# Performance work log

Hardware: AMD Instinct MI355X
Metric: run time of the kernel (lower is better)

## Reference

```python
import jax, jax.numpy as jnp
import numpy as np

EPS = 1e-6
NUM_HEADS = 16

def _phi(x):
    # elu kernel feature map: elu(x) + 1 (ensures positivity)
    return jax.nn.elu(x) + 1.0

def setup_inputs() -> dict:
    key = jax.random.key(0)
    ks = jax.random.split(key, 5)
    B, S, D = 2, 2048, 1024
    scale = 1.0 / np.sqrt(D)  # mimic xavier-ish magnitude
    return {
        "x": jax.random.normal(ks[0], (B, S, D), dtype=jnp.float32),
        "Wq": jax.random.normal(ks[1], (D, D), dtype=jnp.float32) * scale,
        "bq": jnp.zeros((D,), dtype=jnp.float32),
        "Wk": jax.random.normal(ks[2], (D, D), dtype=jnp.float32) * scale,
        "bk": jnp.zeros((D,), dtype=jnp.float32),
        "Wv": jax.random.normal(ks[3], (D, D), dtype=jnp.float32) * scale,
        "bv": jnp.zeros((D,), dtype=jnp.float32),
        "Wo": jax.random.normal(ks[4], (D, D), dtype=jnp.float32) * scale,
        "bo": jnp.zeros((D,), dtype=jnp.float32),
    }

def reference(x, Wq, bq, Wk, bk, Wv, bv, Wo, bo):
    B, S, D = x.shape
    H = NUM_HEADS
    hd = D // H
    # projections (torch Linear: x @ W.T + b)
    q = (x @ Wq.T + bq).reshape(B, S, H, hd).transpose(0, 2, 1, 3)  # [B,H,S,d]
    k = (x @ Wk.T + bk).reshape(B, S, H, hd).transpose(0, 2, 1, 3)
    v = (x @ Wv.T + bv).reshape(B, S, H, hd).transpose(0, 2, 1, 3)
    q = _phi(q)
    k = _phi(k)
    # prefix sums of outer products k_t v_t^T and of k_t (causal linear attention)
    kv_cum = jnp.cumsum(k[..., :, None] * v[..., None, :], axis=2)  # [B,H,S,d,d]
    k_cum = jnp.cumsum(k, axis=2)                                   # [B,H,S,d]
    num = jnp.einsum('bhsd,bhsde->bhse', q, kv_cum)                 # [B,H,S,d]
    den = jnp.einsum('bhsd,bhsd->bhs', q, k_cum)                    # [B,H,S]
    out = num / (den[..., None] + EPS)
    out = out.transpose(0, 2, 1, 3).reshape(B, S, D)
    return out @ Wo.T + bo
```

## Files before the change

### kernel.cpp

```cpp
#include <hip/hip_runtime.h>

typedef unsigned short u16;
typedef __attribute__((ext_vector_type(8))) short bf16x8;
typedef __attribute__((ext_vector_type(4))) float f32x4;

#define DEVI static __device__ __forceinline__

DEVI u16 f2bf(float f) {
  union { float f; unsigned int u; } a; a.f = f;
  unsigned int u = a.u;
  u += 0x7fffu + ((u >> 16) & 1u);
  return (u16)(u >> 16);
}
DEVI float bf2f(u16 h) {
  union { unsigned int u; float f; } a; a.u = ((unsigned int)h) << 16;
  return a.f;
}

DEVI void gload_lds16(const u16* g, u16* l) {
  __builtin_amdgcn_global_load_lds(
      (const __attribute__((address_space(1))) void*)g,
      (__attribute__((address_space(3))) void*)l, 16, 0, 0);
}

DEVI int ldsIdx(int row, int col) {
  return ((col >> 5) << 11) + (row << 5) + (col & 31);
}

struct alignas(8) US4 { u16 a, b, c, d; };

__global__ __launch_bounds__(256) void k_cvt(const float* __restrict__ s,
                                             u16* __restrict__ d, int n4) {
  int i = blockIdx.x * 256 + threadIdx.x;
  if (i >= n4) return;
  f32x4 v = ((const f32x4*)s)[i];
  US4 o{f2bf(v[0]), f2bf(v[1]), f2bf(v[2]), f2bf(v[3])};
  ((US4*)d)[i] = o;
}

__global__ __launch_bounds__(256) void k_gemm_qkv(
    const u16* __restrict__ A, const u16* __restrict__ W,
    const float* __restrict__ bq, const float* __restrict__ bk,
    const float* __restrict__ bv, u16* __restrict__ qb, u16* __restrict__ kb,
    u16* __restrict__ ktb, u16* __restrict__ vtb) {
  __shared__ __align__(16) u16 As[128 * 32];
  __shared__ __align__(16) u16 Bs[128 * 32];
  const int tid = threadIdx.x;
  const int lane = tid & 63;
  const int wave = tid >> 6;
  const int wm = wave >> 1, wn = wave & 1;
  const int m0 = blockIdx.x * 128, n0 = blockIdx.y * 128;
  const int K = 1024;

  f32x4 acc[4][4];
#pragma unroll
  for (int i = 0; i < 4; i++)
#pragma unroll
    for (int j = 0; j < 4; j++) acc[i][j] = (f32x4){0.f, 0.f, 0.f, 0.f};

  const int r0 = tid >> 2, c0 = (tid & 3) * 8;
  const int r1 = (tid + 256) >> 2;
  const u16* Ab0 = A + (size_t)(m0 + r0) * K + c0;
  const u16* Ab1 = A + (size_t)(m0 + r1) * K + c0;
  const u16* Bb0 = W + (size_t)(n0 + r0) * K + c0;
  const u16* Bb1 = W + (size_t)(n0 + r1) * K + c0;
  u16* lA0 = &As[tid * 8];
  u16* lA1 = &As[(tid + 256) * 8];
  u16* lB0 = &Bs[tid * 8];
  u16* lB1 = &Bs[(tid + 256) * 8];

  for (int k0 = 0; k0 < K; k0 += 32) {
    __syncthreads();
    gload_lds16(Ab0 + k0, lA0);
    gload_lds16(Ab1 + k0, lA1);
    gload_lds16(Bb0 + k0, lB0);
    gload_lds16(Bb1 + k0, lB1);
    __syncthreads();
    const int koff = (lane >> 4) * 8;
    bf16x8 af[4], bfr[4];
#pragma unroll
    for (int t = 0; t < 4; t++) {
      af[t] = *(const bf16x8*)&As[(wm * 64 + t * 16 + (lane & 15)) * 32 + koff];
      bfr[t] = *(const bf16x8*)&Bs[(wn * 64 + t * 16 + (lane & 15)) * 32 + koff];
    }
#pragma unroll
    for (int i = 0; i < 4; i++)
#pragma unroll
      for (int j = 0; j < 4; j++)
        acc[i][j] = __builtin_amdgcn_mfma_f32_16x16x32_bf16(af[i], bfr[j],
                                                            acc[i][j], 0, 0, 0);
  }

  const int lr = (lane >> 4) * 4, lc = lane & 15;
  const int region = (int)(blockIdx.y >> 3);
  const float* bias = region == 0 ? bq : (region == 1 ? bk : bv);
#pragma unroll
  for (int j = 0; j < 4; j++) {
    const int colg = n0 + wn * 64 + j * 16 + lc;
    const int cl = colg - (region << 10);
    const float bvv = bias[cl];
#pragma unroll
    for (int i = 0; i < 4; i++) {
      const int row0 = m0 + wm * 64 + i * 16 + lr;
      float v4[4];
#pragma unroll
      for (int r = 0; r < 4; r++) {
        float v = acc[i][j][r] + bvv;
        if (region < 2) v = (v > 0.f) ? (v + 1.f) : __expf(v);
        v4[r] = v;
      }
      if (region == 0) {
#pragma unroll
        for (int r = 0; r < 4; r++)
          qb[(size_t)(row0 + r) * 1024 + cl] = f2bf(v4[r]);
      } else if (region == 1) {
#pragma unroll
        for (int r = 0; r < 4; r++)
          kb[(size_t)(row0 + r) * 1024 + cl] = f2bf(v4[r]);
        US4 o{f2bf(v4[0]), f2bf(v4[1]), f2bf(v4[2]), f2bf(v4[3])};
        *(US4*)&ktb[(size_t)cl * 4096 + row0] = o;
      } else {
        US4 o{f2bf(v4[0]), f2bf(v4[1]), f2bf(v4[2]), f2bf(v4[3])};
        *(US4*)&vtb[(size_t)cl * 4096 + row0] = o;
      }
    }
  }
}

__global__ __launch_bounds__(256) void k_gemm_out(const u16* __restrict__ A,
                                                  const u16* __restrict__ B,
                                                  const float* __restrict__ bias,
                                                  float* __restrict__ C, int M,
                                                  int N, int K) {
  __shared__ __align__(16) u16 As[128 * 32];
  __shared__ __align__(16) u16 Bs[128 * 32];
  const int tid = threadIdx.x;
  const int lane = tid & 63;
  const int wave = tid >> 6;
  const int wm = wave >> 1, wn = wave & 1;
  const int m0 = blockIdx.x * 128, n0 = blockIdx.y * 128;

  f32x4 acc[4][4];
#pragma unroll
  for (int i = 0; i < 4; i++)
#pragma unroll
    for (int j = 0; j < 4; j++) acc[i][j] = (f32x4){0.f, 0.f, 0.f, 0.f};

  const int r0 = tid >> 2, c0 = (tid & 3) * 8;
  const int r1 = (tid + 256) >> 2;
  const u16* Ab0 = A + (size_t)(m0 + r0) * K + c0;
  const u16* Ab1 = A + (size_t)(m0 + r1) * K + c0;
  const u16* Bb0 = B + (size_t)(n0 + r0) * K + c0;
  const u16* Bb1 = B + (size_t)(n0 + r1) * K + c0;
  u16* lA0 = &As[tid * 8];
  u16* lA1 = &As[(tid + 256) * 8];
  u16* lB0 = &Bs[tid * 8];
  u16* lB1 = &Bs[(tid + 256) * 8];

  for (int k0 = 0; k0 < K; k0 += 32) {
    __syncthreads();
    gload_lds16(Ab0 + k0, lA0);
    gload_lds16(Ab1 + k0, lA1);
    gload_lds16(Bb0 + k0, lB0);
    gload_lds16(Bb1 + k0, lB1);
    __syncthreads();
    const int koff = (lane >> 4) * 8;
    bf16x8 af[4], bfr[4];
#pragma unroll
    for (int t = 0; t < 4; t++) {
      af[t] = *(const bf16x8*)&As[(wm * 64 + t * 16 + (lane & 15)) * 32 + koff];
      bfr[t] = *(const bf16x8*)&Bs[(wn * 64 + t * 16 + (lane & 15)) * 32 + koff];
    }
#pragma unroll
    for (int i = 0; i < 4; i++)
#pragma unroll
      for (int j = 0; j < 4; j++)
        acc[i][j] = __builtin_amdgcn_mfma_f32_16x16x32_bf16(af[i], bfr[j],
                                                            acc[i][j], 0, 0, 0);
  }

  const int lr = (lane >> 4) * 4, lc = lane & 15;
#pragma unroll
  for (int j = 0; j < 4; j++) {
    const int col = n0 + wn * 64 + j * 16 + lc;
    const float bv = bias[col];
#pragma unroll
    for (int i = 0; i < 4; i++) {
      const int row = m0 + wm * 64 + i * 16 + lr;
#pragma unroll
      for (int r = 0; r < 4; r++)
        C[(size_t)(row + r) * N + col] = acc[i][j][r] + bv;
    }
  }
}

__global__ __launch_bounds__(256) void k_chunk2(const u16* __restrict__ ktb,
                                                const u16* __restrict__ vtb,
                                                float* __restrict__ KVt,
                                                float* __restrict__ Ks) {
  __shared__ __align__(16) u16 Kt[4096];
  __shared__ __align__(16) u16 Vt[4096];
  __shared__ float ksp[64][4];
  const int tid = threadIdx.x, lane = tid & 63, wave = tid >> 6;
  const int ci = blockIdx.x, h = blockIdx.y, b = blockIdx.z;
  const int t0 = b * 2048 + ci * 64, dB = h * 64;
  const int c = (b * 16 + h) * 32 + ci;
  const int row = tid >> 2, colr = (tid & 3) * 8;
#pragma unroll
  for (int r = 0; r < 2; r++) {
    const int col = r * 32 + colr;
    gload_lds16(ktb + (size_t)(dB + row) * 4096 + t0 + col, Kt + r * 2048 + tid * 8);
    gload_lds16(vtb + (size_t)(dB + row) * 4096 + t0 + col, Vt + r * 2048 + tid * 8);
  }
  __syncthreads();
  {
    const int rr = tid >> 2, part = tid & 3;
    float s = 0.f;
#pragma unroll
    for (int t = 0; t < 16; t++) s += bf2f(Kt[ldsIdx(rr, part * 16 + t)]);
    ksp[rr][part] = s;
  }
  __syncthreads();
  if (tid < 64)
    Ks[c * 64 + tid] = ksp[tid][0] + ksp[tid][1] + ksp[tid][2] + ksp[tid][3];

  const int wm = wave >> 1, wn = wave & 1;
  const int md0 = wm * 32, ne0 = wn * 32;
  const int m = lane & 15, quad = lane >> 4;
  f32x4 acc[2][2];
#pragma unroll
  for (int i = 0; i < 2; i++)
#pragma unroll
    for (int j = 0; j < 2; j++) acc[i][j] = (f32x4){0.f, 0.f, 0.f, 0.f};
#pragma unroll
  for (int ks = 0; ks < 2; ks++) {
    const int koff = ks * 32 + quad * 8;
    bf16x8 af[2], bfr[2];
#pragma unroll
    for (int i = 0; i < 2; i++)
      af[i] = *(const bf16x8*)&Kt[ldsIdx(md0 + i * 16 + m, koff)];
#pragma unroll
    for (int j = 0; j < 2; j++)
      bfr[j] = *(const bf16x8*)&Vt[ldsIdx(ne0 + j * 16 + m, koff)];
#pragma unroll
    for (int i = 0; i < 2; i++)
#pragma unroll
      for (int j = 0; j < 2; j++)
        acc[i][j] = __builtin_amdgcn_mfma_f32_16x16x32_bf16(af[i], bfr[j],
                                                            acc[i][j], 0, 0, 0);
  }
  float* out = KVt + (size_t)c * 4096;
#pragma unroll
  for (int i = 0; i < 2; i++)
#pragma unroll
    for (int j = 0; j < 2; j++) {
      const int e = ne0 + j * 16 + m;
      const int d0 = md0 + i * 16 + quad * 4;
      *(f32x4*)&out[e * 64 + d0] = acc[i][j];
    }
}

__global__ __launch_bounds__(256) void k_prefix(float* __restrict__ KV,
                                                float* __restrict__ Ks) {
  const int slice = blockIdx.x;
  const int bh = blockIdx.y;
  const int tid = threadIdx.x;
  float* base = KV + (size_t)bh * 32 * 4096 + slice * 512;
  float r0 = 0.f, r1 = 0.f;
  for (int ci = 0; ci < 32; ci++) {
    float* p = base + ci * 4096;
    float v0 = p[tid];
    float v1 = p[tid + 256];
    p[tid] = r0;
    p[tid + 256] = r1;
    r0 += v0;
    r1 += v1;
  }
  if (slice == 0 && tid < 64) {
    float* zb = Ks + bh * 32 * 64;
    float zr = 0.f;
    for (int ci = 0; ci < 32; ci++) {
      float v = zb[ci * 64 + tid];
      zb[ci * 64 + tid] = zr;
      zr += v;
    }
  }
}

__global__ __launch_bounds__(256) void k_attn2(const u16* __restrict__ qb,
                                               const u16* __restrict__ kb,
                                               const u16* __restrict__ vtb,
                                               const float* __restrict__ KVt,
                                               const float* __restrict__ Ksg,
                                               u16* __restrict__ Og) {
  __shared__ __align__(16) u16 Qs[4096];
  __shared__ __align__(16) u16 Kr[4096];
  __shared__ __align__(16) u16 Vt[4096];
  __shared__ __align__(16) u16 St[4096];
  __shared__ __align__(16) u16 Am[64 * 72];
  __shared__ float denp[64][4];
  __shared__ float den[64];
  __shared__ float zc[64];
  const int tid = threadIdx.x, lane = tid & 63, wave = tid >> 6;
  const int ci = blockIdx.x, h = blockIdx.y, b = blockIdx.z;
  const int t0 = b * 2048 + ci * 64, colb = h * 64;
  const int c = (b * 16 + h) * 32 + ci;
  const int row = tid >> 2, colr = (tid & 3) * 8;
#pragma unroll
  for (int r = 0; r < 2; r++) {
    const int col = r * 32 + colr;
    gload_lds16(qb + (size_t)(t0 + row) * 1024 + colb + col, Qs + r * 2048 + tid * 8);
    gload_lds16(kb + (size_t)(t0 + row) * 1024 + colb + col, Kr + r * 2048 + tid * 8);
    gload_lds16(vtb + (size_t)(colb + row) * 4096 + t0 + col, Vt + r * 2048 + tid * 8);
  }
  const float* Sp = KVt + (size_t)c * 4096;
#pragma unroll
  for (int jj = 0; jj < 4; jj++) {
    const int off = (tid + jj * 256) * 4;
    f32x4 v = *(const f32x4*)&Sp[off];
    const int e = off >> 6, dd = off & 63;
    US4 o{f2bf(v[0]), f2bf(v[1]), f2bf(v[2]), f2bf(v[3])};
    *(US4*)&St[ldsIdx(e, dd)] = o;
  }
  if (tid < 16) *(f32x4*)&zc[tid * 4] = *(const f32x4*)&Ksg[c * 64 + tid * 4];
  __syncthreads();

  const int wm = wave >> 1, wn = wave & 1;
  const int tm0 = wm * 32, sn0 = wn * 32;
  const int m = lane & 15, quad = lane >> 4;

  f32x4 accA[2][2];
#pragma unroll
  for (int i = 0; i < 2; i++)
#pragma unroll
    for (int j = 0; j < 2; j++) accA[i][j] = (f32x4){0.f, 0.f, 0.f, 0.f};
#pragma unroll
  for (int ks = 0; ks < 2; ks++) {
    const int koff = ks * 32 + quad * 8;
    bf16x8 af[2], bfr[2];
#pragma unroll
    for (int i = 0; i < 2; i++)
      af[i] = *(const bf16x8*)&Qs[ldsIdx(tm0 + i * 16 + m, koff)];
#pragma unroll
    for (int j = 0; j < 2; j++)
      bfr[j] = *(const bf16x8*)&Kr[ldsIdx(sn0 + j * 16 + m, koff)];
#pragma unroll
    for (int i = 0; i < 2; i++)
#pragma unroll
      for (int j = 0; j < 2; j++)
        accA[i][j] = __builtin_amdgcn_mfma_f32_16x16x32_bf16(af[i], bfr[j],
                                                             accA[i][j], 0, 0, 0);
  }
#pragma unroll
  for (int i = 0; i < 2; i++)
#pragma unroll
    for (int j = 0; j < 2; j++) {
      const int s = sn0 + j * 16 + m;
#pragma unroll
      for (int r = 0; r < 4; r++) {
        const int t = tm0 + i * 16 + quad * 4 + r;
        const float v = (s <= t) ? accA[i][j][r] : 0.f;
        Am[t * 72 + s] = f2bf(v);
      }
    }
  __syncthreads();
  {
    const int rr = tid >> 2, part = tid & 3;
    float rs = 0.f, qz = 0.f;
#pragma unroll
    for (int s = 0; s < 16; s++) rs += bf2f(Am[rr * 72 + part * 16 + s]);
#pragma unroll
    for (int d = 0; d < 16; d++)
      qz += bf2f(Qs[ldsIdx(rr, part * 16 + d)]) * zc[part * 16 + d];
    denp[rr][part] = rs + qz;
  }
  __syncthreads();
  if (tid < 64)
    den[tid] =
        denp[tid][0] + denp[tid][1] + denp[tid][2] + denp[tid][3] + 1e-6f;
  __syncthreads();

  f32x4 accO[2][2];
#pragma unroll
  for (int i = 0; i < 2; i++)
#pragma unroll
    for (int j = 0; j < 2; j++) accO[i][j] = (f32x4){0.f, 0.f, 0.f, 0.f};
#pragma unroll
  for (int ks = 0; ks < 2; ks++) {
    const int koff = ks * 32 + quad * 8;
    bf16x8 afA[2], bfV[2], afQ[2], bfS[2];
#pragma unroll
    for (int i = 0; i < 2; i++) {
      afA[i] = *(const bf16x8*)&Am[(tm0 + i * 16 + m) * 72 + koff];
      afQ[i] = *(const bf16x8*)&Qs[ldsIdx(tm0 + i * 16 + m, koff)];
    }
#pragma unroll
    for (int j = 0; j < 2; j++) {
      bfV[j] = *(const bf16x8*)&Vt[ldsIdx(sn0 + j * 16 + m, koff)];
      bfS[j] = *(const bf16x8*)&St[ldsIdx(sn0 + j * 16 + m, koff)];
    }
#pragma unroll
    for (int i = 0; i < 2; i++)
#pragma unroll
      for (int j = 0; j < 2; j++) {
        accO[i][j] = __builtin_amdgcn_mfma_f32_16x16x32_bf16(afA[i], bfV[j],
                                                             accO[i][j], 0, 0, 0);
        accO[i][j] = __builtin_amdgcn_mfma_f32_16x16x32_bf16(afQ[i], bfS[j],
                                                             accO[i][j], 0, 0, 0);
      }
  }
#pragma unroll
  for (int i = 0; i < 2; i++)
#pragma unroll
    for (int r = 0; r < 4; r++) {
      const int t = tm0 + i * 16 + quad * 4 + r;
      const float inv = 1.f / den[t];
#pragma unroll
      for (int j = 0; j < 2; j++) {
        const int e = sn0 + j * 16 + m;
        Og[(size_t)(t0 + t) * 1024 + colb + e] = f2bf(accO[i][j][r] * inv);
      }
    }
}

extern "C" void kernel_launch(void* const* d_in, const int* in_sizes, int n_in,
                              void* d_out, int out_size, void* d_ws,
                              size_t ws_size, hipStream_t stream) {
  const float* x = (const float*)d_in[0];
  const float* Wq = (const float*)d_in[1];
  const float* bq = (const float*)d_in[2];
  const float* Wk = (const float*)d_in[3];
  const float* bk = (const float*)d_in[4];
  const float* Wv = (const float*)d_in[5];
  const float* bv = (const float*)d_in[6];
  const float* Wo = (const float*)d_in[7];
  const float* bo = (const float*)d_in[8];

  char* ws = (char*)d_ws;
  u16* xb = (u16*)(ws + 0);
  u16* ab = xb;
  u16* Wqb = (u16*)(ws + 8388608);
  u16* Wob = (u16*)(ws + 14680064);
  u16* qb = (u16*)(ws + 16777216);
  u16* kb = (u16*)(ws + 25165824);
  u16* ktb = (u16*)(ws + 33554432);
  u16* vtb = (u16*)(ws + 41943040);
  float* KVt = (float*)(ws + 50331648);
  float* Ks = (float*)(ws + 67108864);

  k_cvt<<<4096, 256, 0, stream>>>(x, xb, 1048576);
  k_cvt<<<1024, 256, 0, stream>>>(Wq, Wqb, 262144);
  k_cvt<<<1024, 256, 0, stream>>>(Wk, (u16*)(ws + 10485760), 262144);
  k_cvt<<<1024, 256, 0, stream>>>(Wv, (u16*)(ws + 12582912), 262144);
  k_cvt<<<1024, 256, 0, stream>>>(Wo, Wob, 262144);

  k_gemm_qkv<<<dim3(32, 24), 256, 0, stream>>>(xb, Wqb, bq, bk, bv, qb, kb,
                                               ktb, vtb);

  dim3 ga(32, 16, 2);
  k_chunk2<<<ga, 256, 0, stream>>>(ktb, vtb, KVt, Ks);
  k_prefix<<<dim3(8, 32), 256, 0, stream>>>(KVt, Ks);
  k_attn2<<<ga, 256, 0, stream>>>(qb, kb, vtb, KVt, Ks, ab);

  k_gemm_out<<<dim3(32, 8), 256, 0, stream>>>(ab, Wob, bo, (float*)d_out, 4096,
                                              1024, 1024);
}
```

Baseline: 184.7 us.

## Fuse conversion launches, deepen GEMM K-tile, store chunk KV state in bf16

Merges the five fp32-to-bf16 conversion launches into one kernel. Both GEMMs now load a 64-wide K slab per barrier pair, halving the number of synchronisations. The per-chunk KV states are written as bf16 through an LDS staging tile, so the prefix scan moves half the bytes and the attention kernel can DMA them straight into LDS. The scan also batches all loads into registers up front. The cost is a bf16 rounding of the running KV prefix sums, which loses accuracy, and a doubled shared-memory footprint in the GEMMs that may lower occupancy.

```diff
diff --git a/kernel.cpp b/kernel.cpp
--- a/kernel.cpp
+++ b/kernel.cpp
@@ -29,13 +29,27 @@
 
 struct alignas(8) US4 { u16 a, b, c, d; };
 
-__global__ __launch_bounds__(256) void k_cvt(const float* __restrict__ s,
-                                             u16* __restrict__ d, int n4) {
+__global__ __launch_bounds__(256) void k_cvt_all(
+    const float* __restrict__ x, const float* __restrict__ Wq,
+    const float* __restrict__ Wk, const float* __restrict__ Wv,
+    const float* __restrict__ Wo, u16* __restrict__ xb, u16* __restrict__ Wqb,
+    u16* __restrict__ Wkb, u16* __restrict__ Wvb, u16* __restrict__ Wob) {
   int i = blockIdx.x * 256 + threadIdx.x;
-  if (i >= n4) return;
-  f32x4 v = ((const f32x4*)s)[i];
+  const float* s;
+  u16* d;
+  int off;
+  if (i < 1048576) {
+    s = x; d = xb; off = i;
+  } else {
+    int j = i - 1048576;
+    int w = j >> 18;
+    off = j & 262143;
+    s = (w == 0) ? Wq : (w == 1) ? Wk : (w == 2) ? Wv : Wo;
+    d = (w == 0) ? Wqb : (w == 1) ? Wkb : (w == 2) ? Wvb : Wob;
+  }
+  f32x4 v = ((const f32x4*)s)[off];
   US4 o{f2bf(v[0]), f2bf(v[1]), f2bf(v[2]), f2bf(v[3])};
-  ((US4*)d)[i] = o;
+  ((US4*)d)[off] = o;
 }
 
 __global__ __launch_bounds__(256) void k_gemm_qkv(
@@ -43,14 +57,15 @@
     const float* __restrict__ bq, const float* __restrict__ bk,
     const float* __restrict__ bv, u16* __restrict__ qb, u16* __restrict__ kb,
     u16* __restrict__ ktb, u16* __restrict__ vtb) {
-  __shared__ __align__(16) u16 As[128 * 32];
-  __shared__ __align__(16) u16 Bs[128 * 32];
+  __shared__ __align__(16) u16 As[8192];
+  __shared__ __align__(16) u16 Bs[8192];
   const int tid = threadIdx.x;
   const int lane = tid & 63;
   const int wave = tid >> 6;
   const int wm = wave >> 1, wn = wave & 1;
   const int m0 = blockIdx.x * 128, n0 = blockIdx.y * 128;
   const int K = 1024;
+  const int m = lane & 15, quad = lane >> 4;
 
   f32x4 acc[4][4];
 #pragma unroll
@@ -58,40 +73,47 @@
 #pragma unroll
     for (int j = 0; j < 4; j++) acc[i][j] = (f32x4){0.f, 0.f, 0.f, 0.f};
 
-  const int r0 = tid >> 2, c0 = (tid & 3) * 8;
-  const int r1 = (tid + 256) >> 2;
-  const u16* Ab0 = A + (size_t)(m0 + r0) * K + c0;
-  const u16* Ab1 = A + (size_t)(m0 + r1) * K + c0;
-  const u16* Bb0 = W + (size_t)(n0 + r0) * K + c0;
-  const u16* Bb1 = W + (size_t)(n0 + r1) * K + c0;
-  u16* lA0 = &As[tid * 8];
-  u16* lA1 = &As[(tid + 256) * 8];
-  u16* lB0 = &Bs[tid * 8];
-  u16* lB1 = &Bs[(tid + 256) * 8];
-
-  for (int k0 = 0; k0 < K; k0 += 32) {
+  const u16* Ap[4];
+  const u16* Bp[4];
+  u16* lA[4];
+  u16* lB[4];
+#pragma unroll
+  for (int t = 0; t < 4; t++) {
+    const int s = tid + t * 256;
+    const int rr = (s >> 2) & 127;
+    const int cc = ((s >> 9) << 5) + (tid & 3) * 8;
+    Ap[t] = A + (size_t)(m0 + rr) * K + cc;
+    Bp[t] = W + (size_t)(n0 + rr) * K + cc;
+    lA[t] = &As[s * 8];
+    lB[t] = &Bs[s * 8];
+  }
+
+  for (int k0 = 0; k0 < K; k0 += 64) {
     __syncthreads();
-    gload_lds16(Ab0 + k0, lA0);
-    gload_lds16(Ab1 + k0, lA1);
-    gload_lds16(Bb0 + k0, lB0);
-    gload_lds16(Bb1 + k0, lB1);
+#pragma unroll
+    for (int t = 0; t < 4; t++) gload_lds16(Ap[t] + k0, lA[t]);
+#pragma unroll
+    for (int t = 0; t < 4; t++) gload_lds16(Bp[t] + k0, lB[t]);
     __syncthreads();
-    const int koff = (lane >> 4) * 8;
-    bf16x8 af[4], bfr[4];
-#pragma unroll
-    for (int t = 0; t < 4; t++) {
-      af[t] = *(const bf16x8*)&As[(wm * 64 + t * 16 + (lane & 15)) * 32 + koff];
-      bfr[t] = *(const bf16x8*)&Bs[(wn * 64 + t * 16 + (lane & 15)) * 32 + koff];
-    }
-#pragma unroll
-    for (int i = 0; i < 4; i++)
-#pragma unroll
-      for (int j = 0; j < 4; j++)
-        acc[i][j] = __builtin_amdgcn_mfma_f32_16x16x32_bf16(af[i], bfr[j],
-                                                            acc[i][j], 0, 0, 0);
-  }
-
-  const int lr = (lane >> 4) * 4, lc = lane & 15;
+#pragma unroll
+    for (int kk = 0; kk < 2; kk++) {
+      const int koff = kk * 4096 + quad * 8;
+      bf16x8 af[4], bfr[4];
+#pragma unroll
+      for (int t = 0; t < 4; t++) {
+        af[t] = *(const bf16x8*)&As[(wm * 64 + t * 16 + m) * 32 + koff];
+        bfr[t] = *(const bf16x8*)&Bs[(wn * 64 + t * 16 + m) * 32 + koff];
+      }
+#pragma unroll
+      for (int i = 0; i < 4; i++)
+#pragma unroll
+        for (int j = 0; j < 4; j++)
+          acc[i][j] = __builtin_amdgcn_mfma_f32_16x16x32_bf16(af[i], bfr[j],
+                                                              acc[i][j], 0, 0, 0);
+    }
+  }
+
+  const int lr = quad * 4, lc = m;
   const int region = (int)(blockIdx.y >> 3);
   const float* bias = region == 0 ? bq : (region == 1 ? bk : bv);
 #pragma unroll
@@ -132,13 +154,14 @@
                                                   const float* __restrict__ bias,
                                                   float* __restrict__ C, int M,
                                                   int N, int K) {
-  __shared__ __align__(16) u16 As[128 * 32];
-  __shared__ __align__(16) u16 Bs[128 * 32];
+  __shared__ __align__(16) u16 As[8192];
+  __shared__ __align__(16) u16 Bs[8192];
   const int tid = threadIdx.x;
   const int lane = tid & 63;
   const int wave = tid >> 6;
   const int wm = wave >> 1, wn = wave & 1;
   const int m0 = blockIdx.x * 128, n0 = blockIdx.y * 128;
+  const int m = lane & 15, quad = lane >> 4;
 
   f32x4 acc[4][4];
 #pragma unroll
@@ -146,40 +169,47 @@
 #pragma unroll
     for (int j = 0; j < 4; j++) acc[i][j] = (f32x4){0.f, 0.f, 0.f, 0.f};
 
-  const int r0 = tid >> 2, c0 = (tid & 3) * 8;
-  const int r1 = (tid + 256) >> 2;
-  const u16* Ab0 = A + (size_t)(m0 + r0) * K + c0;
-  const u16* Ab1 = A + (size_t)(m0 + r1) * K + c0;
-  const u16* Bb0 = B + (size_t)(n0 + r0) * K + c0;
-  const u16* Bb1 = B + (size_t)(n0 + r1) * K + c0;
-  u16* lA0 = &As[tid * 8];
-  u16* lA1 = &As[(tid + 256) * 8];
-  u16* lB0 = &Bs[tid * 8];
-  u16* lB1 = &Bs[(tid + 256) * 8];
-
-  for (int k0 = 0; k0 < K; k0 += 32) {
+  const u16* Ap[4];
+  const u16* Bp[4];
+  u16* lA[4];
+  u16* lB[4];
+#pragma unroll
+  for (int t = 0; t < 4; t++) {
+    const int s = tid + t * 256;
+    const int rr = (s >> 2) & 127;
+    const int cc = ((s >> 9) << 5) + (tid & 3) * 8;
+    Ap[t] = A + (size_t)(m0 + rr) * K + cc;
+    Bp[t] = B + (size_t)(n0 + rr) * K + cc;
+    lA[t] = &As[s * 8];
+    lB[t] = &Bs[s * 8];
+  }
+
+  for (int k0 = 0; k0 < K; k0 += 64) {
     __syncthreads();
-    gload_lds16(Ab0 + k0, lA0);
-    gload_lds16(Ab1 + k0, lA1);
-    gload_lds16(Bb0 + k0, lB0);
-    gload_lds16(Bb1 + k0, lB1);
+#pragma unroll
+    for (int t = 0; t < 4; t++) gload_lds16(Ap[t] + k0, lA[t]);
+#pragma unroll
+    for (int t = 0; t < 4; t++) gload_lds16(Bp[t] + k0, lB[t]);
     __syncthreads();
-    const int koff = (lane >> 4) * 8;
-    bf16x8 af[4], bfr[4];
-#pragma unroll
-    for (int t = 0; t < 4; t++) {
-      af[t] = *(const bf16x8*)&As[(wm * 64 + t * 16 + (lane & 15)) * 32 + koff];
-      bfr[t] = *(const bf16x8*)&Bs[(wn * 64 + t * 16 + (lane & 15)) * 32 + koff];
-    }
-#pragma unroll
-    for (int i = 0; i < 4; i++)
-#pragma unroll
-      for (int j = 0; j < 4; j++)
-        acc[i][j] = __builtin_amdgcn_mfma_f32_16x16x32_bf16(af[i], bfr[j],
-                                                            acc[i][j], 0, 0, 0);
-  }
-
-  const int lr = (lane >> 4) * 4, lc = lane & 15;
+#pragma unroll
+    for (int kk = 0; kk < 2; kk++) {
+      const int koff = kk * 4096 + quad * 8;
+      bf16x8 af[4], bfr[4];
+#pragma unroll
+      for (int t = 0; t < 4; t++) {
+        af[t] = *(const bf16x8*)&As[(wm * 64 + t * 16 + m) * 32 + koff];
+        bfr[t] = *(const bf16x8*)&Bs[(wn * 64 + t * 16 + m) * 32 + koff];
+      }
+#pragma unroll
+      for (int i = 0; i < 4; i++)
+#pragma unroll
+        for (int j = 0; j < 4; j++)
+          acc[i][j] = __builtin_amdgcn_mfma_f32_16x16x32_bf16(af[i], bfr[j],
+                                                              acc[i][j], 0, 0, 0);
+    }
+  }
+
+  const int lr = quad * 4, lc = m;
 #pragma unroll
   for (int j = 0; j < 4; j++) {
     const int col = n0 + wn * 64 + j * 16 + lc;
@@ -196,10 +226,11 @@
 
 __global__ __launch_bounds__(256) void k_chunk2(const u16* __restrict__ ktb,
                                                 const u16* __restrict__ vtb,
-                                                float* __restrict__ KVt,
+                                                u16* __restrict__ KVtb,
                                                 float* __restrict__ Ks) {
   __shared__ __align__(16) u16 Kt[4096];
   __shared__ __align__(16) u16 Vt[4096];
+  __shared__ __align__(16) u16 Ct[64 * 72];
   __shared__ float ksp[64][4];
   const int tid = threadIdx.x, lane = tid & 63, wave = tid >> 6;
   const int ci = blockIdx.x, h = blockIdx.y, b = blockIdx.z;
@@ -249,40 +280,57 @@
         acc[i][j] = __builtin_amdgcn_mfma_f32_16x16x32_bf16(af[i], bfr[j],
                                                             acc[i][j], 0, 0, 0);
   }
-  float* out = KVt + (size_t)c * 4096;
 #pragma unroll
   for (int i = 0; i < 2; i++)
 #pragma unroll
     for (int j = 0; j < 2; j++) {
       const int e = ne0 + j * 16 + m;
       const int d0 = md0 + i * 16 + quad * 4;
-      *(f32x4*)&out[e * 64 + d0] = acc[i][j];
-    }
-}
-
-__global__ __launch_bounds__(256) void k_prefix(float* __restrict__ KV,
+      US4 o{f2bf(acc[i][j][0]), f2bf(acc[i][j][1]), f2bf(acc[i][j][2]),
+            f2bf(acc[i][j][3])};
+      *(US4*)&Ct[e * 72 + d0] = o;
+    }
+  __syncthreads();
+  u16* outp = KVtb + (size_t)c * 4096;
+#pragma unroll
+  for (int rd = 0; rd < 2; rd++) {
+    const int g0 = (tid + rd * 256) * 8;
+    const int e = g0 >> 6, d = g0 & 63;
+    bf16x8 v = *(const bf16x8*)&Ct[e * 72 + d];
+    *(bf16x8*)&outp[g0] = v;
+  }
+}
+
+__global__ __launch_bounds__(256) void k_prefix(u16* __restrict__ KVtb,
                                                 float* __restrict__ Ks) {
   const int slice = blockIdx.x;
   const int bh = blockIdx.y;
   const int tid = threadIdx.x;
-  float* base = KV + (size_t)bh * 32 * 4096 + slice * 512;
+  u16* base = KVtb + (size_t)bh * 32 * 4096 + slice * 512 + tid * 2;
+  unsigned int vals[32];
+#pragma unroll
+  for (int ci = 0; ci < 32; ci++)
+    vals[ci] = *(const unsigned int*)(base + ci * 4096);
   float r0 = 0.f, r1 = 0.f;
+#pragma unroll
   for (int ci = 0; ci < 32; ci++) {
-    float* p = base + ci * 4096;
-    float v0 = p[tid];
-    float v1 = p[tid + 256];
-    p[tid] = r0;
-    p[tid + 256] = r1;
+    const float v0 = bf2f((u16)(vals[ci] & 0xffffu));
+    const float v1 = bf2f((u16)(vals[ci] >> 16));
+    const unsigned int o = (unsigned int)f2bf(r0) | ((unsigned int)f2bf(r1) << 16);
+    *(unsigned int*)(base + ci * 4096) = o;
     r0 += v0;
     r1 += v1;
   }
   if (slice == 0 && tid < 64) {
-    float* zb = Ks + bh * 32 * 64;
+    float* p = Ks + (size_t)bh * 32 * 64 + tid;
+    float zb[32];
+#pragma unroll
+    for (int ci = 0; ci < 32; ci++) zb[ci] = p[ci * 64];
     float zr = 0.f;
+#pragma unroll
     for (int ci = 0; ci < 32; ci++) {
-      float v = zb[ci * 64 + tid];
-      zb[ci * 64 + tid] = zr;
-      zr += v;
+      p[ci * 64] = zr;
+      zr += zb[ci];
     }
   }
 }
@@ -290,7 +338,7 @@
 __global__ __launch_bounds__(256) void k_attn2(const u16* __restrict__ qb,
                                                const u16* __restrict__ kb,
                                                const u16* __restrict__ vtb,
-                                               const float* __restrict__ KVt,
+                                               const u16* __restrict__ KVtb,
                                                const float* __restrict__ Ksg,
                                                u16* __restrict__ Og) {
   __shared__ __align__(16) u16 Qs[4096];
@@ -312,15 +360,7 @@
     gload_lds16(qb + (size_t)(t0 + row) * 1024 + colb + col, Qs + r * 2048 + tid * 8);
     gload_lds16(kb + (size_t)(t0 + row) * 1024 + colb + col, Kr + r * 2048 + tid * 8);
     gload_lds16(vtb + (size_t)(colb + row) * 4096 + t0 + col, Vt + r * 2048 + tid * 8);
-  }
-  const float* Sp = KVt + (size_t)c * 4096;
-#pragma unroll
-  for (int jj = 0; jj < 4; jj++) {
-    const int off = (tid + jj * 256) * 4;
-    f32x4 v = *(const f32x4*)&Sp[off];
-    const int e = off >> 6, dd = off & 63;
-    US4 o{f2bf(v[0]), f2bf(v[1]), f2bf(v[2]), f2bf(v[3])};
-    *(US4*)&St[ldsIdx(e, dd)] = o;
+    gload_lds16(KVtb + (size_t)c * 4096 + row * 64 + col, St + r * 2048 + tid * 8);
   }
   if (tid < 16) *(f32x4*)&zc[tid * 4] = *(const f32x4*)&Ksg[c * 64 + tid * 4];
   __syncthreads();
@@ -440,27 +480,26 @@
   u16* xb = (u16*)(ws + 0);
   u16* ab = xb;
   u16* Wqb = (u16*)(ws + 8388608);
+  u16* Wkb = (u16*)(ws + 10485760);
+  u16* Wvb = (u16*)(ws + 12582912);
   u16* Wob = (u16*)(ws + 14680064);
   u16* qb = (u16*)(ws + 16777216);
   u16* kb = (u16*)(ws + 25165824);
   u16* ktb = (u16*)(ws + 33554432);
   u16* vtb = (u16*)(ws + 41943040);
-  float* KVt = (float*)(ws + 50331648);
-  float* Ks = (float*)(ws + 67108864);
-
-  k_cvt<<<4096, 256, 0, stream>>>(x, xb, 1048576);
-  k_cvt<<<1024, 256, 0, stream>>>(Wq, Wqb, 262144);
-  k_cvt<<<1024, 256, 0, stream>>>(Wk, (u16*)(ws + 10485760), 262144);
-  k_cvt<<<1024, 256, 0, stream>>>(Wv, (u16*)(ws + 12582912), 262144);
-  k_cvt<<<1024, 256, 0, stream>>>(Wo, Wob, 262144);
+  u16* KVtb = (u16*)(ws + 50331648);
+  float* Ks = (float*)(ws + 58720256);
+
+  k_cvt_all<<<8192, 256, 0, stream>>>(x, Wq, Wk, Wv, Wo, xb, Wqb, Wkb, Wvb,
+                                      Wob);
 
   k_gemm_qkv<<<dim3(32, 24), 256, 0, stream>>>(xb, Wqb, bq, bk, bv, qb, kb,
                                                ktb, vtb);
 
   dim3 ga(32, 16, 2);
-  k_chunk2<<<ga, 256, 0, stream>>>(ktb, vtb, KVt, Ks);
-  k_prefix<<<dim3(8, 32), 256, 0, stream>>>(KVt, Ks);
-  k_attn2<<<ga, 256, 0, stream>>>(qb, kb, vtb, KVt, Ks, ab);
+  k_chunk2<<<ga, 256, 0, stream>>>(ktb, vtb, KVtb, Ks);
+  k_prefix<<<dim3(8, 32), 256, 0, stream>>>(KVtb, Ks);
+  k_attn2<<<ga, 256, 0, stream>>>(qb, kb, vtb, KVtb, Ks, ab);
 
   k_gemm_out<<<dim3(32, 8), 256, 0, stream>>>(ab, Wob, bo, (float*)d_out, 4096,
                                               1024, 1024);
```

Measured after the change: 180.0 us. 1.03x faster.
